# Kernel optimization log

Hardware: AMD Instinct MI355X
Metric: run time of the kernel (lower is better)

The kernel has to match this reference:

```python
import jax, jax.numpy as jnp
import numpy as np

N, E, R = 50000, 500000, 3
IN, HID, OUT = 128, 128, 128
NEG_SLOPE = 0.2


def setup_inputs() -> dict:
    key = jax.random.key(0)
    ks = jax.random.split(key, 16)
    g = lambda i, shape: jax.random.normal(ks[i], shape, jnp.float32) * 0.1
    return {
        "x": jax.random.normal(ks[0], (N, IN), jnp.float32),
        "edge_index": jax.random.randint(ks[1], (2, E), 0, N, jnp.int32),
        "edge_type": jax.random.randint(ks[2], (E,), 0, R, jnp.int32),
        "edge_attr": jax.random.normal(ks[3], (E, 1), jnp.float32),
        # conv1 params (RGATConv: per-relation weight, q/k/e attention vectors, edge lin, bias)
        "w1": g(4, (R, IN, HID)), "q1": g(5, (HID, 1)), "k1": g(6, (HID, 1)),
        "le1": g(7, (1, HID)), "e1": g(8, (HID, 1)), "b1": jnp.zeros((HID,), jnp.float32),
        # conv2 params
        "w2": g(9, (R, HID, OUT)), "q2": g(10, (OUT, 1)), "k2": g(11, (OUT, 1)),
        "le2": g(12, (1, OUT)), "e2": g(13, (OUT, 1)), "b2": jnp.zeros((OUT,), jnp.float32),
    }


def _rgat_conv(x, src, dst, edge_type, edge_attr, w, q, k, le, e, b):
    """PyG RGATConv: heads=1, dim=1, additive-self-attention, across-relation softmax."""
    n = x.shape[0]
    # Per-relation linear at node level (equiv. to per-edge bmm with w[edge_type])
    xw = jnp.einsum('ni,rio->rno', x, w)            # [R, N, C]
    x_j = xw[edge_type, src]                          # [E, C] transformed source feats
    x_i = xw[edge_type, dst]                          # [E, C] transformed target feats
    # additive attention logits: q(x_i) + k(x_j) + e(lin_edge(edge_attr))
    alpha = x_i @ q + x_j @ k + (edge_attr @ le) @ e  # [E, 1]
    alpha = jax.nn.leaky_relu(alpha, negative_slope=NEG_SLOPE)
    # across-relation softmax over incoming edges of each target node
    amax = jax.ops.segment_max(alpha, dst, num_segments=n)
    amax = jnp.where(jnp.isfinite(amax), amax, 0.0)   # empty segments -> 0
    ex = jnp.exp(alpha - amax[dst])
    denom = jax.ops.segment_sum(ex, dst, num_segments=n)
    alpha = ex / (denom[dst] + 1e-16)
    # weighted scatter-add aggregation, then bias (concat=True, heads=1)
    out = jax.ops.segment_sum(alpha * x_j, dst, num_segments=n)  # [N, C]
    return out + b


def reference(x, edge_index, edge_type, edge_attr,
              w1, q1, k1, le1, e1, b1,
              w2, q2, k2, le2, e2, b2):
    src, dst = edge_index[0], edge_index[1]
    h = jax.nn.relu(_rgat_conv(x, src, dst, edge_type, edge_attr, w1, q1, k1, le1, e1, b1))
    return _rgat_conv(h, src, dst, edge_type, edge_attr, w2, q2, k2, le2, e2, b2)
```

## Files before the change

### kernel.cpp

```cpp
#include <hip/hip_runtime.h>
#include <hip/hip_bf16.h>
#include <math.h>

typedef __bf16 bf16x8 __attribute__((ext_vector_type(8)));
typedef float f32x4 __attribute__((ext_vector_type(4)));

#define CDIM 128
#define ECAP 192

__global__ void sentinel_kernel(float* outf) {
  if (threadIdx.x == 0) outf[0] = 12345.0f;
}

__global__ __launch_bounds__(256) void prep_kernel(
    const float* __restrict__ w1, const float* __restrict__ w2,
    __hip_bfloat16* __restrict__ wt,
    const float* __restrict__ le1, const float* __restrict__ e1,
    const float* __restrict__ le2, const float* __restrict__ e2,
    float* __restrict__ outc, int perW) {
  if (blockIdx.x == gridDim.x - 1) {
    __shared__ float s1[128], s2[128];
    int t = threadIdx.x;
    if (t < 128) { s1[t] = le1[t] * e1[t]; s2[t] = le2[t] * e2[t]; }
    __syncthreads();
    for (int off = 64; off > 0; off >>= 1) {
      if (t < off) { s1[t] += s1[t + off]; s2[t] += s2[t + off]; }
      __syncthreads();
    }
    if (t == 0) { outc[0] = s1[0]; outc[1] = s2[0]; }
    return;
  }
  int t = blockIdx.x * 256 + threadIdx.x;
  if (t >= perW * 2) return;
  const float* w = (t < perW) ? w1 : w2;
  int tt = (t < perW) ? t : t - perW;
  int r = tt >> 11;
  int rem = tt & 2047;
  int kb = rem >> 7;
  int o = rem & 127;
  const float* wr = w + ((size_t)r << 14);
  union { __hip_bfloat16 h[8]; int4 v; } u;
#pragma unroll
  for (int j = 0; j < 8; ++j)
    u.h[j] = __float2bfloat16(wr[(size_t)(kb * 8 + j) * CDIM + o]);
  *reinterpret_cast<int4*>(wt + (size_t)t * 8) = u.v;
}


__global__ __launch_bounds__(256) void hist_kernel(const int* __restrict__ dstv,
                                                   int* __restrict__ deg, int E) {
  int e = blockIdx.x * 256 + threadIdx.x;
  if (e < E) atomicAdd(&deg[dstv[e]], 1);
}

__global__ __launch_bounds__(256) void scan1_kernel(const int* __restrict__ deg,
                                                    int* __restrict__ rowptr,
                                                    int* __restrict__ partials, int n) {
  __shared__ int sh[256];
  int t = threadIdx.x;
  int base = blockIdx.x * 1024;
  int idx = base + t * 4;
  int v[4]; int s = 0;
#pragma unroll
  for (int j = 0; j < 4; ++j) { v[j] = (idx + j < n) ? deg[idx + j] : 0; s += v[j]; }
  sh[t] = s;
  __syncthreads();
  for (int off = 1; off < 256; off <<= 1) {
    int x = (t >= off) ? sh[t - off] : 0;
    __syncthreads();
    sh[t] += x;
    __syncthreads();
  }
  int excl = sh[t] - s;
  if (t == 255) partials[blockIdx.x] = sh[255];
  int run = excl;
#pragma unroll
  for (int j = 0; j < 4; ++j) {
    if (idx + j < n) rowptr[idx + j] = run;
    run += v[j];
  }
}

__global__ __launch_bounds__(256) void scan2_kernel(int* __restrict__ partials, int nb) {
  __shared__ int sh[256];
  int carry = 0;
  for (int base = 0; base < nb; base += 256) {
    int i = base + threadIdx.x;
    int v = (i < nb) ? partials[i] : 0;
    sh[threadIdx.x] = v;
    __syncthreads();
    for (int off = 1; off < 256; off <<= 1) {
      int x = (threadIdx.x >= off) ? sh[threadIdx.x - off] : 0;
      __syncthreads();
      sh[threadIdx.x] += x;
      __syncthreads();
    }
    if (i < nb) partials[i] = carry + sh[threadIdx.x] - v;
    carry += sh[255];
    __syncthreads();
  }
}

__global__ __launch_bounds__(256) void scan3_kernel(int* __restrict__ rowptr,
                                                    int* __restrict__ cursor,
                                                    const int* __restrict__ partials,
                                                    int n, int E) {
  int i = blockIdx.x * 256 + threadIdx.x;
  if (i < n) {
    int v = rowptr[i] + partials[i >> 10];
    rowptr[i] = v;
    cursor[i] = v;
  } else if (i == n) {
    rowptr[n] = E;
  }
}

__global__ __launch_bounds__(256) void scatter_kernel(
    const int* __restrict__ srcv, const int* __restrict__ dstv,
    const int* __restrict__ etype, const float* __restrict__ eattr,
    int* __restrict__ cursor, int2* __restrict__ kattr, int E, int n) {
  int e = blockIdx.x * 256 + threadIdx.x;
  if (e >= E) return;
  int p = atomicAdd(&cursor[dstv[e]], 1);
  kattr[p] = make_int2(etype[e] * n + srcv[e], __float_as_int(eattr[e]));
}

__global__ __launch_bounds__(256) void gemm_xw_kernel(
    const float* __restrict__ xin, const __hip_bfloat16* __restrict__ wt,
    const float* __restrict__ qv, const float* __restrict__ kv,
    __hip_bfloat16* __restrict__ xwout, float* __restrict__ sq, float* __restrict__ sk,
    int n) {
  __shared__ __hip_bfloat16 wlds[16 * 128 * 8];
  const int r = blockIdx.y;
  const int base = blockIdx.x * 128;
  const int tid = threadIdx.x;
  {
    const int4* src = reinterpret_cast<const int4*>(wt + ((size_t)r << 14));
    int4* dst = reinterpret_cast<int4*>(wlds);
    for (int i = tid; i < 2048; i += 256) dst[i] = src[i];
  }
  __syncthreads();

  const int wave = tid >> 6, lane = tid & 63;
  const int quad = lane >> 4, c16 = lane & 15;

  bf16x8 zf;
#pragma unroll
  for (int j = 0; j < 8; ++j) zf[j] = (__bf16)0.0f;

  bf16x8 af[2][4];
#pragma unroll
  for (int h = 0; h < 2; ++h) {
    int m = base + wave * 32 + h * 16 + c16;
#pragma unroll
    for (int ks = 0; ks < 4; ++ks) {
      if (m < n) {
        const float* xp = xin + (size_t)m * CDIM + ks * 32 + quad * 8;
        f32x4 x0 = *reinterpret_cast<const f32x4*>(xp);
        f32x4 x1 = *reinterpret_cast<const f32x4*>(xp + 4);
        bf16x8 a;
#pragma unroll
        for (int j = 0; j < 4; ++j) { a[j] = (__bf16)x0[j]; a[4 + j] = (__bf16)x1[j]; }
        af[h][ks] = a;
      } else {
        af[h][ks] = zf;
      }
    }
  }

  f32x4 acc[2][8];
#pragma unroll
  for (int h = 0; h < 2; ++h)
#pragma unroll
    for (int nt = 0; nt < 8; ++nt) acc[h][nt] = (f32x4){0.f, 0.f, 0.f, 0.f};

#pragma unroll
  for (int ks = 0; ks < 4; ++ks) {
#pragma unroll
    for (int nt = 0; nt < 8; ++nt) {
      bf16x8 b = *reinterpret_cast<const bf16x8*>(
          &wlds[(((ks * 4 + quad) * 128) + nt * 16 + c16) * 8]);
      acc[0][nt] = __builtin_amdgcn_mfma_f32_16x16x32_bf16(af[0][ks], b, acc[0][nt], 0, 0, 0);
      acc[1][nt] = __builtin_amdgcn_mfma_f32_16x16x32_bf16(af[1][ks], b, acc[1][nt], 0, 0, 0);
    }
  }

  float qf[8], kf[8];
#pragma unroll
  for (int nt = 0; nt < 8; ++nt) {
    qf[nt] = qv[nt * 16 + c16];
    kf[nt] = kv[nt * 16 + c16];
  }

#pragma unroll
  for (int h = 0; h < 2; ++h) {
    int rowb = base + wave * 32 + h * 16 + quad * 4;
#pragma unroll
    for (int reg = 0; reg < 4; ++reg) {
      int grow = rowb + reg;
      float s_q = 0.f, s_k = 0.f;
#pragma unroll
      for (int nt = 0; nt < 8; ++nt) {
        float v = acc[h][nt][reg];
        if (grow < n)
          xwout[(((size_t)r * n + grow) << 7) + nt * 16 + c16] = __float2bfloat16(v);
        s_q += v * qf[nt];
        s_k += v * kf[nt];
      }
#pragma unroll
      for (int off = 1; off < 16; off <<= 1) {
        s_q += __shfl_xor(s_q, off, 64);
        s_k += __shfl_xor(s_k, off, 64);
      }
      if (c16 == 0 && grow < n) {
        sq[r * n + grow] = s_q;
        sk[r * n + grow] = s_k;
      }
    }
  }
}

__global__ __launch_bounds__(256) void aggregate_kernel(
    const int* __restrict__ rowptr, const int2* __restrict__ kattr,
    const float* __restrict__ sq, const float* __restrict__ sk,
    const __hip_bfloat16* __restrict__ xw, const float* __restrict__ bias,
    const float* __restrict__ cscal, float* __restrict__ out, int n, int do_relu) {
  __shared__ int2 ldsE[4][ECAP];
  const int wave = threadIdx.x >> 6, lane = threadIdx.x & 63;
  const int node = blockIdx.x * 4 + wave;
  const bool active = node < n;
  const float c = cscal[0];
  const int n2 = n * 2;

  int start = 0, deg = 0;
  float s0 = 0.f, s1 = 0.f, s2 = 0.f;
  if (active) {
    start = rowptr[node];
    deg = rowptr[node + 1] - start;
    s0 = sq[node]; s1 = sq[n + node]; s2 = sq[n2 + node];
  }

  float m = -__builtin_inff();
  if (active) {
    for (int j = lane; j < deg; j += 64) {
      int2 ka = kattr[start + j];
      int kk = ka.x;
      float sv = (kk >= n2) ? s2 : ((kk >= n) ? s1 : s0);
      float l = sv + sk[kk] + c * __int_as_float(ka.y);
      l = l > 0.f ? l : 0.2f * l;
      if (j < ECAP) ldsE[wave][j] = make_int2(kk, __float_as_int(l));
      m = fmaxf(m, l);
    }
  }
#pragma unroll
  for (int off = 32; off > 0; off >>= 1) m = fmaxf(m, __shfl_xor(m, off, 64));
  __syncthreads();

  const int cap = deg < ECAP ? deg : ECAP;
  if (active) {
    for (int i = lane; i < cap; i += 64) {
      int2 e = ldsE[wave][i];
      e.y = __float_as_int(__expf(__int_as_float(e.y) - m));
      ldsE[wave][i] = e;
    }
  }
  __syncthreads();

  const int g = lane >> 4;
  const int sub = lane & 15;
  float acc[8];
#pragma unroll
  for (int t = 0; t < 8; ++t) acc[t] = 0.f;
  float den = 0.f;

  if (active) {
    for (int j0 = 0; j0 < cap; j0 += 4) {
      int j = j0 + g;
      float w = 0.f; int kk = 0;
      if (j < cap) {
        int2 e = ldsE[wave][j];
        kk = e.x;
        w = __int_as_float(e.y);
      }
      bf16x8 f = *reinterpret_cast<const bf16x8*>(xw + ((size_t)kk << 7) + sub * 8);
#pragma unroll
      for (int t = 0; t < 8; ++t) acc[t] += w * (float)f[t];
      den += w;
    }
    for (int j0 = cap; j0 < deg; j0 += 4) {
      int j = j0 + g;
      float w = 0.f; int kk = 0;
      if (j < deg) {
        int2 ka = kattr[start + j];
        kk = ka.x;
        float sv = (kk >= n2) ? s2 : ((kk >= n) ? s1 : s0);
        float l = sv + sk[kk] + c * __int_as_float(ka.y);
        l = l > 0.f ? l : 0.2f * l;
        w = __expf(l - m);
      }
      bf16x8 f = *reinterpret_cast<const bf16x8*>(xw + ((size_t)kk << 7) + sub * 8);
#pragma unroll
      for (int t = 0; t < 8; ++t) acc[t] += w * (float)f[t];
      den += w;
    }

#pragma unroll
    for (int t = 0; t < 8; ++t) {
      acc[t] += __shfl_xor(acc[t], 16, 64);
      acc[t] += __shfl_xor(acc[t], 32, 64);
    }
    den += __shfl_xor(den, 16, 64);
    den += __shfl_xor(den, 32, 64);

    if (g == 0) {
      float inv = 1.0f / (den + 1e-16f);
      f32x4 b0 = *reinterpret_cast<const f32x4*>(bias + sub * 8);
      f32x4 b1 = *reinterpret_cast<const f32x4*>(bias + sub * 8 + 4);
      f32x4 o0, o1;
#pragma unroll
      for (int t = 0; t < 4; ++t) {
        o0[t] = acc[t] * inv + b0[t];
        o1[t] = acc[4 + t] * inv + b1[t];
      }
      if (do_relu) {
#pragma unroll
        for (int t = 0; t < 4; ++t) {
          o0[t] = fmaxf(o0[t], 0.f);
          o1[t] = fmaxf(o1[t], 0.f);
        }
      }
      float* op = out + (size_t)node * CDIM + sub * 8;
      *reinterpret_cast<f32x4*>(op) = o0;
      *reinterpret_cast<f32x4*>(op + 4) = o1;
    }
  }
}


extern "C" void kernel_launch(void* const* d_in, const int* in_sizes, int n_in,
                              void* d_out, int out_size, void* d_ws, size_t ws_size,
                              hipStream_t stream) {
  const float* x     = (const float*)d_in[0];
  const int*   eidx  = (const int*)d_in[1];
  const int*   etype = (const int*)d_in[2];
  const float* eattr = (const float*)d_in[3];
  const float* w1  = (const float*)d_in[4];
  const float* q1  = (const float*)d_in[5];
  const float* k1  = (const float*)d_in[6];
  const float* le1 = (const float*)d_in[7];
  const float* e1  = (const float*)d_in[8];
  const float* b1  = (const float*)d_in[9];
  const float* w2  = (const float*)d_in[10];
  const float* q2  = (const float*)d_in[11];
  const float* k2  = (const float*)d_in[12];
  const float* le2 = (const float*)d_in[13];
  const float* e2  = (const float*)d_in[14];
  const float* b2  = (const float*)d_in[15];

  const int N = in_sizes[0] / CDIM;
  const int E = in_sizes[2];
  const int R = in_sizes[4] / (CDIM * CDIM);
  const int* srcv = eidx;
  const int* dstv = eidx + E;

  char* p = (char*)d_ws;
  auto alloc = [&](size_t bytes) -> void* {
    void* q = (void*)p;
    p += (bytes + 255) & ~(size_t)255;
    return q;
  };
  float* sq       = (float*)alloc((size_t)R * N * 4);
  float* sk       = (float*)alloc((size_t)R * N * 4);
  int*   deg      = (int*)alloc((size_t)N * 4);
  int*   rowptr   = (int*)alloc((size_t)(N + 1) * 4);
  int*   cursor   = (int*)alloc((size_t)N * 4);
  int*   partials = (int*)alloc(4096);
  int2*  kattr    = (int2*)alloc((size_t)E * 8);
  __hip_bfloat16* wt = (__hip_bfloat16*)alloc((size_t)2 * R * CDIM * CDIM * 2);
  float* cscal    = (float*)alloc(256);
  __hip_bfloat16* xw = (__hip_bfloat16*)alloc((size_t)R * N * CDIM * 2);

  size_t needed = (size_t)(p - (char*)d_ws);
  if (needed > ws_size) {
    sentinel_kernel<<<1, 64, 0, stream>>>((float*)d_out);
    return;
  }

  float* outp = (float*)d_out;
  float* hbuf = outp;

  const int eg = (E + 255) / 256;
  const int nb = (N + 1023) / 1024;
  const int nodes4 = (N + 3) / 4;
  const int perW = R * 2048;

  prep_kernel<<<(perW * 2 + 255) / 256 + 1, 256, 0, stream>>>(
      w1, w2, wt, le1, e1, le2, e2, cscal, perW);

  hipMemsetAsync(deg, 0, (size_t)N * 4, stream);
  hist_kernel<<<eg, 256, 0, stream>>>(dstv, deg, E);
  scan1_kernel<<<nb, 256, 0, stream>>>(deg, rowptr, partials, N);
  scan2_kernel<<<1, 256, 0, stream>>>(partials, nb);
  scan3_kernel<<<(N + 1 + 255) / 256, 256, 0, stream>>>(rowptr, cursor, partials, N, E);
  scatter_kernel<<<eg, 256, 0, stream>>>(srcv, dstv, etype, eattr, cursor, kattr, E, N);

  dim3 ggrid((N + 127) / 128, R);

  gemm_xw_kernel<<<ggrid, 256, 0, stream>>>(x, wt, q1, k1, xw, sq, sk, N);
  aggregate_kernel<<<nodes4, 256, 0, stream>>>(rowptr, kattr, sq, sk, xw, b1,
                                               cscal + 0, hbuf, N, 1);

  gemm_xw_kernel<<<ggrid, 256, 0, stream>>>(hbuf, wt + (size_t)R * CDIM * CDIM,
                                            q2, k2, xw, sq, sk, N);
  aggregate_kernel<<<nodes4, 256, 0, stream>>>(rowptr, kattr, sq, sk, xw, b2,
                                               cscal + 1, outp, N, 0);
}
```

Measured before the change: 279.2 us.

## Fold q/k attention into GEMM via precomputed W·q, W·k and stage output through LDS

Measured after the change: 293.5 us. +5.1%, slower.

```diff
diff --git a/kernel.cpp b/kernel.cpp
--- a/kernel.cpp
+++ b/kernel.cpp
@@ -7,6 +7,7 @@
 
 #define CDIM 128
 #define ECAP 192
+#define CSTRIDE 132
 
 __global__ void sentinel_kernel(float* outf) {
   if (threadIdx.x == 0) outf[0] = 12345.0f;
@@ -14,13 +15,56 @@
 
 __global__ __launch_bounds__(256) void prep_kernel(
     const float* __restrict__ w1, const float* __restrict__ w2,
-    __hip_bfloat16* __restrict__ wt,
+    __hip_bfloat16* __restrict__ wt, __hip_bfloat16* __restrict__ wqk,
+    const float* __restrict__ q1, const float* __restrict__ k1,
+    const float* __restrict__ q2, const float* __restrict__ k2,
     const float* __restrict__ le1, const float* __restrict__ e1,
     const float* __restrict__ le2, const float* __restrict__ e2,
-    float* __restrict__ outc, int perW) {
-  if (blockIdx.x == gridDim.x - 1) {
+    float* __restrict__ outc, int* __restrict__ deg, int perW, int n) {
+  const int b = blockIdx.x;
+  const int tid = threadIdx.x;
+  if (b < 48) {
+    int t = b * 256 + tid;
+    if (t >= perW * 2) return;
+    const float* w = (t < perW) ? w1 : w2;
+    int tt = (t < perW) ? t : t - perW;
+    int r = tt >> 11;
+    int rem = tt & 2047;
+    int kb = rem >> 7;
+    int o = rem & 127;
+    const float* wr = w + ((size_t)r << 14);
+    union { __hip_bfloat16 h[8]; int4 v; } u;
+#pragma unroll
+    for (int j = 0; j < 8; ++j)
+      u.h[j] = __float2bfloat16(wr[(size_t)(kb * 8 + j) * CDIM + o]);
+    *reinterpret_cast<int4*>(wt + (size_t)t * 8) = u.v;
+  } else if (b < 51) {
+    int u = (b - 48) * 256 + tid;
+    if (u >= 768) return;
+    int conv = u / 384;
+    int rem = u % 384;
+    int rr = rem >> 7;
+    int k = rem & 127;
+    const float* w = conv ? w2 : w1;
+    const float* qv = conv ? q2 : q1;
+    const float* kv = conv ? k2 : k1;
+    const float* wrow = w + ((size_t)rr << 14) + (size_t)k * CDIM;
+    float dq = 0.f, dk = 0.f;
+    for (int o = 0; o < CDIM; ++o) {
+      float wv = wrow[o];
+      dq += wv * qv[o];
+      dk += wv * kv[o];
+    }
+    __hip_bfloat16* dst = wqk + (size_t)conv * 6144 + (size_t)rr * 2048;
+    int kb = k >> 3, j = k & 7;
+#pragma unroll
+    for (int col = 0; col < 16; ++col) {
+      float v = (col == 0) ? dq : (col == 1) ? dk : 0.f;
+      dst[(kb * 16 + col) * 8 + j] = __float2bfloat16(v);
+    }
+  } else if (b == 51) {
     __shared__ float s1[128], s2[128];
-    int t = threadIdx.x;
+    int t = tid;
     if (t < 128) { s1[t] = le1[t] * e1[t]; s2[t] = le2[t] * e2[t]; }
     __syncthreads();
     for (int off = 64; off > 0; off >>= 1) {
@@ -28,22 +72,10 @@
       __syncthreads();
     }
     if (t == 0) { outc[0] = s1[0]; outc[1] = s2[0]; }
-    return;
-  }
-  int t = blockIdx.x * 256 + threadIdx.x;
-  if (t >= perW * 2) return;
-  const float* w = (t < perW) ? w1 : w2;
-  int tt = (t < perW) ? t : t - perW;
-  int r = tt >> 11;
-  int rem = tt & 2047;
-  int kb = rem >> 7;
-  int o = rem & 127;
-  const float* wr = w + ((size_t)r << 14);
-  union { __hip_bfloat16 h[8]; int4 v; } u;
-#pragma unroll
-  for (int j = 0; j < 8; ++j)
-    u.h[j] = __float2bfloat16(wr[(size_t)(kb * 8 + j) * CDIM + o]);
-  *reinterpret_cast<int4*>(wt + (size_t)t * 8) = u.v;
+  } else {
+    int i = (b - 52) * 256 + tid;
+    if (i < n) deg[i] = 0;
+  }
 }
 
 
@@ -127,16 +159,16 @@
 
 __global__ __launch_bounds__(256) void gemm_xw_kernel(
     const float* __restrict__ xin, const __hip_bfloat16* __restrict__ wt,
-    const float* __restrict__ qv, const float* __restrict__ kv,
+    const __hip_bfloat16* __restrict__ wqk,
     __hip_bfloat16* __restrict__ xwout, float* __restrict__ sq, float* __restrict__ sk,
     int n) {
-  __shared__ __hip_bfloat16 wlds[16 * 128 * 8];
+  __shared__ __hip_bfloat16 lds[128 * CSTRIDE];
   const int r = blockIdx.y;
   const int base = blockIdx.x * 128;
   const int tid = threadIdx.x;
   {
     const int4* src = reinterpret_cast<const int4*>(wt + ((size_t)r << 14));
-    int4* dst = reinterpret_cast<int4*>(wlds);
+    int4* dst = reinterpret_cast<int4*>(lds);
     for (int i = tid; i < 2048; i += 256) dst[i] = src[i];
   }
   __syncthreads();
@@ -168,53 +200,71 @@
     }
   }
 
-  f32x4 acc[2][8];
-#pragma unroll
-  for (int h = 0; h < 2; ++h)
+  const __hip_bfloat16* wqkr = wqk + (size_t)r * 2048;
+  bf16x8 qkf[4];
+#pragma unroll
+  for (int ks = 0; ks < 4; ++ks)
+    qkf[ks] = *reinterpret_cast<const bf16x8*>(wqkr + ((ks * 4 + quad) * 16 + c16) * 8);
+
+  f32x4 acc[2][8], accqk[2];
+#pragma unroll
+  for (int h = 0; h < 2; ++h) {
+    accqk[h] = (f32x4){0.f, 0.f, 0.f, 0.f};
 #pragma unroll
     for (int nt = 0; nt < 8; ++nt) acc[h][nt] = (f32x4){0.f, 0.f, 0.f, 0.f};
+  }
 
 #pragma unroll
   for (int ks = 0; ks < 4; ++ks) {
 #pragma unroll
     for (int nt = 0; nt < 8; ++nt) {
       bf16x8 b = *reinterpret_cast<const bf16x8*>(
-          &wlds[(((ks * 4 + quad) * 128) + nt * 16 + c16) * 8]);
+          &lds[(((ks * 4 + quad) * 128) + nt * 16 + c16) * 8]);
       acc[0][nt] = __builtin_amdgcn_mfma_f32_16x16x32_bf16(af[0][ks], b, acc[0][nt], 0, 0, 0);
       acc[1][nt] = __builtin_amdgcn_mfma_f32_16x16x32_bf16(af[1][ks], b, acc[1][nt], 0, 0, 0);
     }
-  }
-
-  float qf[8], kf[8];
-#pragma unroll
-  for (int nt = 0; nt < 8; ++nt) {
-    qf[nt] = qv[nt * 16 + c16];
-    kf[nt] = kv[nt * 16 + c16];
+    accqk[0] = __builtin_amdgcn_mfma_f32_16x16x32_bf16(af[0][ks], qkf[ks], accqk[0], 0, 0, 0);
+    accqk[1] = __builtin_amdgcn_mfma_f32_16x16x32_bf16(af[1][ks], qkf[ks], accqk[1], 0, 0, 0);
   }
 
 #pragma unroll
   for (int h = 0; h < 2; ++h) {
     int rowb = base + wave * 32 + h * 16 + quad * 4;
-#pragma unroll
-    for (int reg = 0; reg < 4; ++reg) {
-      int grow = rowb + reg;
-      float s_q = 0.f, s_k = 0.f;
-#pragma unroll
-      for (int nt = 0; nt < 8; ++nt) {
-        float v = acc[h][nt][reg];
-        if (grow < n)
-          xwout[(((size_t)r * n + grow) << 7) + nt * 16 + c16] = __float2bfloat16(v);
-        s_q += v * qf[nt];
-        s_k += v * kf[nt];
-      }
-#pragma unroll
-      for (int off = 1; off < 16; off <<= 1) {
-        s_q += __shfl_xor(s_q, off, 64);
-        s_k += __shfl_xor(s_k, off, 64);
-      }
-      if (c16 == 0 && grow < n) {
-        sq[r * n + grow] = s_q;
-        sk[r * n + grow] = s_k;
+    if (c16 == 0) {
+#pragma unroll
+      for (int reg = 0; reg < 4; ++reg)
+        if (rowb + reg < n) sq[r * n + rowb + reg] = accqk[h][reg];
+    } else if (c16 == 1) {
+#pragma unroll
+      for (int reg = 0; reg < 4; ++reg)
+        if (rowb + reg < n) sk[r * n + rowb + reg] = accqk[h][reg];
+    }
+  }
+
+  __syncthreads();
+#pragma unroll
+  for (int h = 0; h < 2; ++h) {
+    int rl = wave * 32 + h * 16 + quad * 4;
+#pragma unroll
+    for (int nt = 0; nt < 8; ++nt) {
+#pragma unroll
+      for (int reg = 0; reg < 4; ++reg)
+        lds[(rl + reg) * CSTRIDE + nt * 16 + c16] = __float2bfloat16(acc[h][nt][reg]);
+    }
+  }
+  __syncthreads();
+  {
+    int rl = tid >> 1;
+    int half = tid & 1;
+    int grow = base + rl;
+    if (grow < n) {
+      const __hip_bfloat16* src = lds + rl * CSTRIDE + half * 64;
+      __hip_bfloat16* dst = xwout + (((size_t)r * n + grow) << 7) + half * 64;
+#pragma unroll
+      for (int i = 0; i < 8; ++i) {
+        int2 lo = *reinterpret_cast<const int2*>(src + i * 8);
+        int2 hi = *reinterpret_cast<const int2*>(src + i * 8 + 4);
+        *reinterpret_cast<int4*>(dst + i * 8) = make_int4(lo.x, lo.y, hi.x, hi.y);
       }
     }
   }
@@ -376,7 +426,8 @@
   int*   cursor   = (int*)alloc((size_t)N * 4);
   int*   partials = (int*)alloc(4096);
   int2*  kattr    = (int2*)alloc((size_t)E * 8);
-  __hip_bfloat16* wt = (__hip_bfloat16*)alloc((size_t)2 * R * CDIM * CDIM * 2);
+  __hip_bfloat16* wt  = (__hip_bfloat16*)alloc((size_t)2 * R * CDIM * CDIM * 2);
+  __hip_bfloat16* wqk = (__hip_bfloat16*)alloc((size_t)2 * R * 2048 * 2);
   float* cscal    = (float*)alloc(256);
   __hip_bfloat16* xw = (__hip_bfloat16*)alloc((size_t)R * N * CDIM * 2);
 
@@ -393,11 +444,11 @@
   const int nb = (N + 1023) / 1024;
   const int nodes4 = (N + 3) / 4;
   const int perW = R * 2048;
-
-  prep_kernel<<<(perW * 2 + 255) / 256 + 1, 256, 0, stream>>>(
-      w1, w2, wt, le1, e1, le2, e2, cscal, perW);
-
-  hipMemsetAsync(deg, 0, (size_t)N * 4, stream);
+  const int prep_grid = 52 + (N + 255) / 256;
+
+  prep_kernel<<<prep_grid, 256, 0, stream>>>(w1, w2, wt, wqk, q1, k1, q2, k2,
+                                             le1, e1, le2, e2, cscal, deg, perW, N);
+
   hist_kernel<<<eg, 256, 0, stream>>>(dstv, deg, E);
   scan1_kernel<<<nb, 256, 0, stream>>>(deg, rowptr, partials, N);
   scan2_kernel<<<1, 256, 0, stream>>>(partials, nb);
@@ -406,12 +457,12 @@
 
   dim3 ggrid((N + 127) / 128, R);
 
-  gemm_xw_kernel<<<ggrid, 256, 0, stream>>>(x, wt, q1, k1, xw, sq, sk, N);
+  gemm_xw_kernel<<<ggrid, 256, 0, stream>>>(x, wt, wqk, xw, sq, sk, N);
   aggregate_kernel<<<nodes4, 256, 0, stream>>>(rowptr, kattr, sq, sk, xw, b1,
                                                cscal + 0, hbuf, N, 1);
 
   gemm_xw_kernel<<<ggrid, 256, 0, stream>>>(hbuf, wt + (size_t)R * CDIM * CDIM,
-                                            q2, k2, xw, sq, sk, N);
+                                            wqk + (size_t)R * 2048, xw, sq, sk, N);
   aggregate_kernel<<<nodes4, 256, 0, stream>>>(rowptr, kattr, sq, sk, xw, b2,
                                                cscal + 1, outp, N, 0);
 }
```

## Drop softmax max pass in aggregation and fold degree memset into prep kernel

Applied to the files above, without the earlier changes.

New measurement: 274.5 us. No clear change (-1.7%).

```diff
diff --git a/kernel.cpp b/kernel.cpp
--- a/kernel.cpp
+++ b/kernel.cpp
@@ -6,7 +6,6 @@
 typedef float f32x4 __attribute__((ext_vector_type(4)));
 
 #define CDIM 128
-#define ECAP 192
 
 __global__ void sentinel_kernel(float* outf) {
   if (threadIdx.x == 0) outf[0] = 12345.0f;
@@ -17,10 +16,27 @@
     __hip_bfloat16* __restrict__ wt,
     const float* __restrict__ le1, const float* __restrict__ e1,
     const float* __restrict__ le2, const float* __restrict__ e2,
-    float* __restrict__ outc, int perW) {
-  if (blockIdx.x == gridDim.x - 1) {
+    float* __restrict__ outc, int* __restrict__ deg, int perW, int n) {
+  const int b = blockIdx.x;
+  const int tid = threadIdx.x;
+  if (b < 48) {
+    int t = b * 256 + tid;
+    if (t >= perW * 2) return;
+    const float* w = (t < perW) ? w1 : w2;
+    int tt = (t < perW) ? t : t - perW;
+    int r = tt >> 11;
+    int rem = tt & 2047;
+    int kb = rem >> 7;
+    int o = rem & 127;
+    const float* wr = w + ((size_t)r << 14);
+    union { __hip_bfloat16 h[8]; int4 v; } u;
+#pragma unroll
+    for (int j = 0; j < 8; ++j)
+      u.h[j] = __float2bfloat16(wr[(size_t)(kb * 8 + j) * CDIM + o]);
+    *reinterpret_cast<int4*>(wt + (size_t)t * 8) = u.v;
+  } else if (b == 48) {
     __shared__ float s1[128], s2[128];
-    int t = threadIdx.x;
+    int t = tid;
     if (t < 128) { s1[t] = le1[t] * e1[t]; s2[t] = le2[t] * e2[t]; }
     __syncthreads();
     for (int off = 64; off > 0; off >>= 1) {
@@ -28,22 +44,10 @@
       __syncthreads();
     }
     if (t == 0) { outc[0] = s1[0]; outc[1] = s2[0]; }
-    return;
-  }
-  int t = blockIdx.x * 256 + threadIdx.x;
-  if (t >= perW * 2) return;
-  const float* w = (t < perW) ? w1 : w2;
-  int tt = (t < perW) ? t : t - perW;
-  int r = tt >> 11;
-  int rem = tt & 2047;
-  int kb = rem >> 7;
-  int o = rem & 127;
-  const float* wr = w + ((size_t)r << 14);
-  union { __hip_bfloat16 h[8]; int4 v; } u;
-#pragma unroll
-  for (int j = 0; j < 8; ++j)
-    u.h[j] = __float2bfloat16(wr[(size_t)(kb * 8 + j) * CDIM + o]);
-  *reinterpret_cast<int4*>(wt + (size_t)t * 8) = u.v;
+  } else {
+    int i = (b - 49) * 256 + tid;
+    if (i < n) deg[i] = 0;
+  }
 }
 
 
@@ -225,114 +229,67 @@
     const float* __restrict__ sq, const float* __restrict__ sk,
     const __hip_bfloat16* __restrict__ xw, const float* __restrict__ bias,
     const float* __restrict__ cscal, float* __restrict__ out, int n, int do_relu) {
-  __shared__ int2 ldsE[4][ECAP];
   const int wave = threadIdx.x >> 6, lane = threadIdx.x & 63;
   const int node = blockIdx.x * 4 + wave;
-  const bool active = node < n;
+  if (node >= n) return;
+  const int g = lane >> 4;
+  const int sub = lane & 15;
   const float c = cscal[0];
   const int n2 = n * 2;
 
-  int start = 0, deg = 0;
-  float s0 = 0.f, s1 = 0.f, s2 = 0.f;
-  if (active) {
-    start = rowptr[node];
-    deg = rowptr[node + 1] - start;
-    s0 = sq[node]; s1 = sq[n + node]; s2 = sq[n2 + node];
-  }
-
-  float m = -__builtin_inff();
-  if (active) {
-    for (int j = lane; j < deg; j += 64) {
+  const int start = rowptr[node];
+  const int deg = rowptr[node + 1] - start;
+  const float s0 = sq[node], s1 = sq[n + node], s2 = sq[n2 + node];
+
+  float acc[8];
+#pragma unroll
+  for (int t = 0; t < 8; ++t) acc[t] = 0.f;
+  float den = 0.f;
+
+  for (int j0 = 0; j0 < deg; j0 += 4) {
+    int j = j0 + g;
+    if (j < deg) {
       int2 ka = kattr[start + j];
       int kk = ka.x;
       float sv = (kk >= n2) ? s2 : ((kk >= n) ? s1 : s0);
       float l = sv + sk[kk] + c * __int_as_float(ka.y);
       l = l > 0.f ? l : 0.2f * l;
-      if (j < ECAP) ldsE[wave][j] = make_int2(kk, __float_as_int(l));
-      m = fmaxf(m, l);
-    }
-  }
-#pragma unroll
-  for (int off = 32; off > 0; off >>= 1) m = fmaxf(m, __shfl_xor(m, off, 64));
-  __syncthreads();
-
-  const int cap = deg < ECAP ? deg : ECAP;
-  if (active) {
-    for (int i = lane; i < cap; i += 64) {
-      int2 e = ldsE[wave][i];
-      e.y = __float_as_int(__expf(__int_as_float(e.y) - m));
-      ldsE[wave][i] = e;
-    }
-  }
-  __syncthreads();
-
-  const int g = lane >> 4;
-  const int sub = lane & 15;
-  float acc[8];
-#pragma unroll
-  for (int t = 0; t < 8; ++t) acc[t] = 0.f;
-  float den = 0.f;
-
-  if (active) {
-    for (int j0 = 0; j0 < cap; j0 += 4) {
-      int j = j0 + g;
-      float w = 0.f; int kk = 0;
-      if (j < cap) {
-        int2 e = ldsE[wave][j];
-        kk = e.x;
-        w = __int_as_float(e.y);
-      }
+      float w = __expf(l);
       bf16x8 f = *reinterpret_cast<const bf16x8*>(xw + ((size_t)kk << 7) + sub * 8);
 #pragma unroll
       for (int t = 0; t < 8; ++t) acc[t] += w * (float)f[t];
       den += w;
     }
-    for (int j0 = cap; j0 < deg; j0 += 4) {
-      int j = j0 + g;
-      float w = 0.f; int kk = 0;
-      if (j < deg) {
-        int2 ka = kattr[start + j];
-        kk = ka.x;
-        float sv = (kk >= n2) ? s2 : ((kk >= n) ? s1 : s0);
-        float l = sv + sk[kk] + c * __int_as_float(ka.y);
-        l = l > 0.f ? l : 0.2f * l;
-        w = __expf(l - m);
-      }
-      bf16x8 f = *reinterpret_cast<const bf16x8*>(xw + ((size_t)kk << 7) + sub * 8);
-#pragma unroll
-      for (int t = 0; t < 8; ++t) acc[t] += w * (float)f[t];
-      den += w;
-    }
-
-#pragma unroll
-    for (int t = 0; t < 8; ++t) {
-      acc[t] += __shfl_xor(acc[t], 16, 64);
-      acc[t] += __shfl_xor(acc[t], 32, 64);
-    }
-    den += __shfl_xor(den, 16, 64);
-    den += __shfl_xor(den, 32, 64);
-
-    if (g == 0) {
-      float inv = 1.0f / (den + 1e-16f);
-      f32x4 b0 = *reinterpret_cast<const f32x4*>(bias + sub * 8);
-      f32x4 b1 = *reinterpret_cast<const f32x4*>(bias + sub * 8 + 4);
-      f32x4 o0, o1;
+  }
+
+#pragma unroll
+  for (int t = 0; t < 8; ++t) {
+    acc[t] += __shfl_xor(acc[t], 16, 64);
+    acc[t] += __shfl_xor(acc[t], 32, 64);
+  }
+  den += __shfl_xor(den, 16, 64);
+  den += __shfl_xor(den, 32, 64);
+
+  if (g == 0) {
+    float inv = 1.0f / (den + 1e-16f);
+    f32x4 b0 = *reinterpret_cast<const f32x4*>(bias + sub * 8);
+    f32x4 b1 = *reinterpret_cast<const f32x4*>(bias + sub * 8 + 4);
+    f32x4 o0, o1;
+#pragma unroll
+    for (int t = 0; t < 4; ++t) {
+      o0[t] = acc[t] * inv + b0[t];
+      o1[t] = acc[4 + t] * inv + b1[t];
+    }
+    if (do_relu) {
 #pragma unroll
       for (int t = 0; t < 4; ++t) {
-        o0[t] = acc[t] * inv + b0[t];
-        o1[t] = acc[4 + t] * inv + b1[t];
-      }
-      if (do_relu) {
-#pragma unroll
-        for (int t = 0; t < 4; ++t) {
-          o0[t] = fmaxf(o0[t], 0.f);
-          o1[t] = fmaxf(o1[t], 0.f);
-        }
-      }
-      float* op = out + (size_t)node * CDIM + sub * 8;
-      *reinterpret_cast<f32x4*>(op) = o0;
-      *reinterpret_cast<f32x4*>(op + 4) = o1;
-    }
+        o0[t] = fmaxf(o0[t], 0.f);
+        o1[t] = fmaxf(o1[t], 0.f);
+      }
+    }
+    float* op = out + (size_t)node * CDIM + sub * 8;
+    *reinterpret_cast<f32x4*>(op) = o0;
+    *reinterpret_cast<f32x4*>(op + 4) = o1;
   }
 }
 
@@ -393,11 +350,11 @@
   const int nb = (N + 1023) / 1024;
   const int nodes4 = (N + 3) / 4;
   const int perW = R * 2048;
-
-  prep_kernel<<<(perW * 2 + 255) / 256 + 1, 256, 0, stream>>>(
-      w1, w2, wt, le1, e1, le2, e2, cscal, perW);
-
-  hipMemsetAsync(deg, 0, (size_t)N * 4, stream);
+  const int prep_grid = 49 + (N + 255) / 256;
+
+  prep_kernel<<<prep_grid, 256, 0, stream>>>(w1, w2, wt, le1, e1, le2, e2,
+                                             cscal, deg, perW, N);
+
   hist_kernel<<<eg, 256, 0, stream>>>(dstv, deg, E);
   scan1_kernel<<<nb, 256, 0, stream>>>(deg, rowptr, partials, N);
   scan2_kernel<<<1, 256, 0, stream>>>(partials, nb);
```
